# Kernel tuning notes

Measured on AMD Instinct MI355X. Metric: run time of the kernel, lower is better.

Reference implementation:

```python
import jax, jax.numpy as jnp
import numpy as np

B, N, D, K = 32, 4096, 256, 128


def setup_inputs() -> dict:
    key = jax.random.key(0)
    k1, k2, k3 = jax.random.split(key, 3)
    x = jax.random.normal(k1, (B, N, D), dtype=jnp.float32)
    # 'orthogonal' init proxy: unit-variance-ish codewords
    codewords = jax.random.normal(k2, (K, D), dtype=jnp.float32) / np.float32(np.sqrt(D))
    # keras 'uniform' initializer default range (-0.05, 0.05)
    scale = jax.random.uniform(k3, (K,), dtype=jnp.float32, minval=-0.05, maxval=0.05)
    return {"x": x, "codewords": codewords, "scale": scale}


def reference(x, codewords, scale):
    """Deep-TEN Encoding layer.

    scaledL2: w_ik = S_k * ||x_i - c_k||^2   (expanded, avoids (B,N,K,D) residuals)
    weights : W = softmax_k(w_ik)
    aggregate: E_k = sum_i W_ik * (x_i - c_k)
    """
    x2 = jnp.sum(x * x, axis=-1)                    # (B, N)
    c2 = jnp.sum(codewords * codewords, axis=-1)    # (K,)
    xc = jnp.einsum('bnd,kd->bnk', x, codewords)    # (B, N, K)
    sl2 = scale * (x2[..., None] - 2.0 * xc + c2)   # (B, N, K)
    W = jax.nn.softmax(sl2, axis=-1)                # softmax over codewords K
    # E_k = sum_i W_ik x_i - (sum_i W_ik) c_k
    E = jnp.einsum('bnk,bnd->bkd', W, x) - jnp.sum(W, axis=1)[..., None] * codewords
    return E  # (B, K, D)
```

## Files before the change

### kernel.cpp

```cpp
#include <hip/hip_runtime.h>

#define DEV __device__ __forceinline__

typedef __attribute__((ext_vector_type(8))) short bf16x8;
typedef __attribute__((ext_vector_type(4))) float f32x4;

constexpr int Nn = 4096, Dd = 256, Kk = 128;
constexpr int SEGS = 32;
constexpr int CH2  = 8;
constexpr int NCH  = Nn / CH2;
constexpr int NSTEP = 64;

DEV unsigned short f2bf(float f) {
  unsigned int u = __builtin_bit_cast(unsigned int, f);
  u += 0x7FFFu + ((u >> 16) & 1u);
  return (unsigned short)(u >> 16);
}
DEV float bf2f(unsigned short h) {
  unsigned int u = (unsigned int)h << 16;
  return __builtin_bit_cast(float, u);
}

DEV unsigned lds2(unsigned d, unsigned nbyte) {
  unsigned hh = (d & 7u) ^ ((d >> 4) & 7u) ^ (((d >> 7) & 1u) << 1);
  return d * 128u + (nbyte ^ (hh << 4));
}

DEV unsigned ldsc(unsigned row, unsigned byteInRow) {
  return row * 512u + (byteInRow ^ ((row & 7u) << 4));
}

DEV unsigned ldsw(unsigned k, unsigned nbyte) {
  unsigned h = (k & 7u) ^ (((k >> 3) & 1u) << 1);
  return k * 256u + (nbyte ^ (h << 4));
}

__global__ void enc_prep(const float* __restrict__ cw, const float* __restrict__ sc,
                         unsigned short* __restrict__ cbf, float2* __restrict__ tab,
                         float* __restrict__ Wsumg) {
  int k = blockIdx.x, l = threadIdx.x;
  float4 u = *(const float4*)(cw + k * Dd + l * 4);
  float s2 = u.x * u.x + u.y * u.y + u.z * u.z + u.w * u.w;
  #pragma unroll
  for (int o = 1; o < 64; o <<= 1) s2 += __shfl_xor(s2, o);
  unsigned short* dst = cbf + k * Dd + l * 4;
  dst[0] = f2bf(u.x); dst[1] = f2bf(u.y); dst[2] = f2bf(u.z); dst[3] = f2bf(u.w);
  if (l == 0) { float s = sc[k]; tab[k] = make_float2(s * s2, 2.0f * s); }
  if (l < 32) Wsumg[l * Kk + k] = 0.0f;
}

__global__ __launch_bounds__(512, 1) void enc_w(
    const float* __restrict__ x, const unsigned short* __restrict__ cbf,
    const float2* __restrict__ tab, unsigned short* __restrict__ Wt,
    float* __restrict__ Wsumg) {
  __shared__ __align__(16) char cL[65536];
  __shared__ float2 tabL[Kk];
  __shared__ float WsL[Kk];
  const int tid = threadIdx.x;
  const int w  = tid >> 6;
  const int l  = tid & 63;
  const int g  = l >> 4;
  const int ln = l & 15;

  {
    const int r = tid >> 2, part = tid & 3;
    const char* src = (const char*)cbf + r * 512 + part * 128;
    #pragma unroll
    for (int j = 0; j < 8; ++j) {
      float4 v = *(const float4*)(src + j * 16);
      *(float4*)(cL + ldsc((unsigned)r, (unsigned)(part * 128 + j * 16))) = v;
    }
  }
  if (tid < Kk) { tabL[tid] = tab[tid]; WsL[tid] = 0.0f; }
  __syncthreads();

  const int b   = blockIdx.x >> 5;
  const int seg = blockIdx.x & 31;
  const int nrow = seg * 128 + w * 16 + ln;
  const float* xrow = x + ((size_t)b * Nn + nrow) * Dd;

  f32x4 s1[8];
  const f32x4 zero4 = {0.f, 0.f, 0.f, 0.f};
  #pragma unroll
  for (int f = 0; f < 8; ++f) s1[f] = zero4;
  float x2p = 0.f;

  float4 pu[8][2];
  #pragma unroll
  for (int p = 0; p < 8; ++p) {
    pu[p][0] = *(const float4*)(xrow + p * 32 + g * 8);
    pu[p][1] = *(const float4*)(xrow + p * 32 + g * 8 + 4);
  }

  #pragma unroll
  for (int ks = 0; ks < 8; ++ks) {
    float4 u0 = pu[ks][0], u1 = pu[ks][1];
    x2p += u0.x*u0.x + u0.y*u0.y + u0.z*u0.z + u0.w*u0.w
         + u1.x*u1.x + u1.y*u1.y + u1.z*u1.z + u1.w*u1.w;
    bf16x8 xv;
    xv[0] = (short)f2bf(u0.x); xv[1] = (short)f2bf(u0.y);
    xv[2] = (short)f2bf(u0.z); xv[3] = (short)f2bf(u0.w);
    xv[4] = (short)f2bf(u1.x); xv[5] = (short)f2bf(u1.y);
    xv[6] = (short)f2bf(u1.z); xv[7] = (short)f2bf(u1.w);
    const unsigned colb = (unsigned)(ks * 64 + g * 16);
    #pragma unroll
    for (int f = 0; f < 8; ++f) {
      bf16x8 a = *(const bf16x8*)(cL + ldsc((unsigned)(f * 16 + ln), colb));
      s1[f] = __builtin_amdgcn_mfma_f32_16x16x32_bf16(a, xv, s1[f], 0, 0, 0);
    }
  }

  x2p += __shfl_xor(x2p, 16); x2p += __shfl_xor(x2p, 32);
  const float hx2 = 0.5f * x2p;
  float ssum = 0.f;
  #pragma unroll
  for (int f = 0; f < 8; ++f) {
    #pragma unroll
    for (int r = 0; r < 4; ++r) {
      const float2 ab = tabL[f * 16 + g * 4 + r];
      const float ev = __expf(ab.x + ab.y * (hx2 - s1[f][r]));
      s1[f][r] = ev;
      ssum += ev;
    }
  }
  ssum += __shfl_xor(ssum, 16); ssum += __shfl_xor(ssum, 32);
  const float rinv = 1.0f / ssum;

  __syncthreads();
  #pragma unroll
  for (int f = 0; f < 8; ++f) {
    #pragma unroll
    for (int r = 0; r < 4; ++r) {
      const int cwi = f * 16 + g * 4 + r;
      *(unsigned short*)(cL + ldsw((unsigned)cwi, (unsigned)((w * 16 + ln) * 2)))
          = f2bf(s1[f][r] * rinv);
    }
  }
  __syncthreads();
  {
    char* wq = (char*)(Wt + (size_t)b * Kk * Nn + seg * 128);
    #pragma unroll
    for (int j = 0; j < 4; ++j) {
      const unsigned o = (unsigned)tid * 16u + (unsigned)j * 8192u;
      const unsigned k = o >> 8, nb = o & 255u;
      float4 v = *(const float4*)(cL + ldsw(k, nb));
      *(float4*)(wq + (size_t)k * (Nn * 2) + nb) = v;
      const unsigned short* hv = (const unsigned short*)&v;
      float wsp = 0.f;
      #pragma unroll
      for (int q = 0; q < 8; ++q) wsp += bf2f(hv[q]);
      atomicAdd(&WsL[k], wsp);
    }
  }
  __syncthreads();
  if (tid < Kk) atomicAdd(&Wsumg[b * Kk + tid], WsL[tid]);
}

template<int PM>
__global__ __launch_bounds__(1024) void enc_e(
    const float* __restrict__ x, const unsigned short* __restrict__ Wt,
    unsigned short* __restrict__ Ep, float* __restrict__ out) {
  __shared__ __align__(16) char xs[2 * 32768];

  const int tid = threadIdx.x;
  const int w  = tid >> 6;
  const int l  = tid & 63;
  const int g  = l >> 4;
  const int ln = l & 15;
  const int wr = w >> 2, wc = w & 3;
  const int b  = blockIdx.x >> 3, ch = blockIdx.x & 7;

  const float* xb = x + ((size_t)b * Nn + ch * NCH) * Dd;
  const unsigned short* Wb = Wt + (size_t)b * Kk * Nn + ch * NCH;

  const int srow = w * 4 + g;
  const int sd0  = ln * 16;

  f32x4 acc[2][4];
  const f32x4 zero4 = {0.f, 0.f, 0.f, 0.f};
  #pragma unroll
  for (int mi = 0; mi < 2; ++mi)
    #pragma unroll
    for (int ni = 0; ni < 4; ++ni) acc[mi][ni] = zero4;

  {
    const float* p = xb + (size_t)srow * Dd + sd0;
    float4 u0 = *(const float4*)(p + 0), u1 = *(const float4*)(p + 4);
    float4 u2 = *(const float4*)(p + 8), u3 = *(const float4*)(p + 12);
    const float uu[16] = {u0.x,u0.y,u0.z,u0.w, u1.x,u1.y,u1.z,u1.w,
                          u2.x,u2.y,u2.z,u2.w, u3.x,u3.y,u3.z,u3.w};
    #pragma unroll
    for (int j = 0; j < 16; ++j)
      *(unsigned short*)(xs + lds2((unsigned)(sd0 + j), (unsigned)(srow * 2))) = f2bf(uu[j]);
  }
  bf16x8 wf[2][2];
  #pragma unroll
  for (int ks2 = 0; ks2 < 2; ++ks2)
    #pragma unroll
    for (int mi = 0; mi < 2; ++mi)
      wf[ks2][mi] = *(const bf16x8*)(Wb + (size_t)(wr * 32 + mi * 16 + ln) * Nn
                                        + ks2 * 32 + g * 8);
  __syncthreads();

  int cur = 0;
  for (int s = 0; s < CH2; ++s) {
    float4 n0, n1, n2, n3;
    bf16x8 wn[2][2];
    if (s + 1 < CH2) {
      const float* p = xb + (size_t)((s + 1) * NSTEP + srow) * Dd + sd0;
      n0 = *(const float4*)(p + 0); n1 = *(const float4*)(p + 4);
      n2 = *(const float4*)(p + 8); n3 = *(const float4*)(p + 12);
      #pragma unroll
      for (int ks2 = 0; ks2 < 2; ++ks2)
        #pragma unroll
        for (int mi = 0; mi < 2; ++mi)
          wn[ks2][mi] = *(const bf16x8*)(Wb + (size_t)(wr * 32 + mi * 16 + ln) * Nn
                                            + (s + 1) * NSTEP + ks2 * 32 + g * 8);
    }

    const char* xcur = xs + (cur << 15);
    #pragma unroll
    for (int ks2 = 0; ks2 < 2; ++ks2) {
      bf16x8 bg[4];
      #pragma unroll
      for (int ni = 0; ni < 4; ++ni)
        bg[ni] = *(const bf16x8*)(xcur + lds2((unsigned)(wc * 64 + ni * 16 + ln),
                                              (unsigned)((ks2 * 32 + g * 8) * 2)));
      #pragma unroll
      for (int mi = 0; mi < 2; ++mi)
        #pragma unroll
        for (int ni = 0; ni < 4; ++ni)
          acc[mi][ni] = __builtin_amdgcn_mfma_f32_16x16x32_bf16(wf[ks2][mi], bg[ni], acc[mi][ni], 0, 0, 0);
    }

    if (s + 1 < CH2) {
      char* xn = xs + ((cur ^ 1) << 15);
      const float uu[16] = {n0.x,n0.y,n0.z,n0.w, n1.x,n1.y,n1.z,n1.w,
                            n2.x,n2.y,n2.z,n2.w, n3.x,n3.y,n3.z,n3.w};
      #pragma unroll
      for (int j = 0; j < 16; ++j)
        *(unsigned short*)(xn + lds2((unsigned)(sd0 + j), (unsigned)(srow * 2))) = f2bf(uu[j]);
      #pragma unroll
      for (int ks2 = 0; ks2 < 2; ++ks2)
        #pragma unroll
        for (int mi = 0; mi < 2; ++mi)
          wf[ks2][mi] = wn[ks2][mi];
    }
    __syncthreads();
    cur ^= 1;
  }

  #pragma unroll
  for (int mi = 0; mi < 2; ++mi) {
    #pragma unroll
    for (int r = 0; r < 4; ++r) {
      const int k = wr * 32 + mi * 16 + g * 4 + r;
      #pragma unroll
      for (int ni = 0; ni < 4; ++ni) {
        const int d = wc * 64 + ni * 16 + ln;
        if (PM == 0) {
          Ep[(size_t)blockIdx.x * (Kk * Dd) + k * Dd + d] = f2bf(acc[mi][ni][r]);
        } else {
          atomicAdd(out + (size_t)b * (Kk * Dd) + k * Dd + d, acc[mi][ni][r]);
        }
      }
    }
  }
}

__global__ __launch_bounds__(256, 1) void enc_reduce_b16(
    const unsigned short* __restrict__ Ep, const float* __restrict__ Wsumg,
    const float* __restrict__ cw, float* __restrict__ out) {
  const size_t i = ((size_t)blockIdx.x * 256 + threadIdx.x) * 16;
  const int b   = (int)(i / (Kk * Dd));
  const int rem = (int)(i % (Kk * Dd));
  const int k   = rem >> 8;
  const unsigned short* p = Ep + (size_t)b * CH2 * (Kk * Dd) + rem;
  const float wsv = Wsumg[b * Kk + k];
  float sx[16];
  #pragma unroll
  for (int j = 0; j < 16; ++j) sx[j] = 0.f;
  #pragma unroll
  for (int c = 0; c < CH2; ++c) {
    const ushort4* q = (const ushort4*)(p + (size_t)c * (Kk * Dd));
    ushort4 v0 = q[0], v1 = q[1], v2 = q[2], v3 = q[3];
    sx[0]  += bf2f(v0.x); sx[1]  += bf2f(v0.y); sx[2]  += bf2f(v0.z); sx[3]  += bf2f(v0.w);
    sx[4]  += bf2f(v1.x); sx[5]  += bf2f(v1.y); sx[6]  += bf2f(v1.z); sx[7]  += bf2f(v1.w);
    sx[8]  += bf2f(v2.x); sx[9]  += bf2f(v2.y); sx[10] += bf2f(v2.z); sx[11] += bf2f(v2.w);
    sx[12] += bf2f(v3.x); sx[13] += bf2f(v3.y); sx[14] += bf2f(v3.z); sx[15] += bf2f(v3.w);
  }
  const float* cp = cw + (size_t)rem;
  float4 c0 = *(const float4*)(cp + 0), c1 = *(const float4*)(cp + 4);
  float4 c2 = *(const float4*)(cp + 8), c3 = *(const float4*)(cp + 12);
  float4* o = (float4*)(out + i);
  o[0] = make_float4(sx[0] - wsv * c0.x, sx[1] - wsv * c0.y, sx[2] - wsv * c0.z, sx[3] - wsv * c0.w);
  o[1] = make_float4(sx[4] - wsv * c1.x, sx[5] - wsv * c1.y, sx[6] - wsv * c1.z, sx[7] - wsv * c1.w);
  o[2] = make_float4(sx[8] - wsv * c2.x, sx[9] - wsv * c2.y, sx[10] - wsv * c2.z, sx[11] - wsv * c2.w);
  o[3] = make_float4(sx[12] - wsv * c3.x, sx[13] - wsv * c3.y, sx[14] - wsv * c3.z, sx[15] - wsv * c3.w);
}

__global__ __launch_bounds__(256, 1) void enc_fix(
    const float* __restrict__ Wsumg, const float* __restrict__ cw,
    float* __restrict__ out) {
  const size_t i = ((size_t)blockIdx.x * 256 + threadIdx.x) * 16;
  const int b   = (int)(i / (Kk * Dd));
  const int rem = (int)(i % (Kk * Dd));
  const int k   = rem >> 8;
  const float wsv = Wsumg[b * Kk + k];
  float* o = out + i;
  const float* cp = cw + (size_t)rem;
  #pragma unroll
  for (int j = 0; j < 16; ++j) o[j] -= wsv * cp[j];
}

extern "C" void kernel_launch(void* const* d_in, const int* in_sizes, int n_in,
                              void* d_out, int out_size, void* d_ws, size_t ws_size,
                              hipStream_t stream) {
  const float* x  = (const float*)d_in[0];
  const float* cw = (const float*)d_in[1];
  const float* sc = (const float*)d_in[2];
  float* out = (float*)d_out;

  unsigned short* cbf = (unsigned short*)d_ws;
  float2* tab = (float2*)((char*)d_ws + 65536);
  float*  Wsumg = (float*)((char*)d_ws + 66560);
  unsigned short* Wt = (unsigned short*)((char*)d_ws + 82944);
  unsigned short* Ep = (unsigned short*)((char*)d_ws + 82944 + (size_t)32 * Kk * Nn * 2);
  const size_t KD = (size_t)Kk * Dd;
  const size_t needFull = 82944 + (size_t)32 * Kk * Nn * 2 + (size_t)32 * CH2 * KD * 2;
  const size_t needAtm  = 82944 + (size_t)32 * Kk * Nn * 2;

  enc_prep<<<dim3(Kk), dim3(64), 0, stream>>>(cw, sc, cbf, tab, Wsumg);
  enc_w<<<dim3(32 * SEGS), dim3(512), 0, stream>>>(x, cbf, tab, Wt, Wsumg);

  if (ws_size >= needFull) {
    enc_e<0><<<dim3(32 * CH2), dim3(1024), 0, stream>>>(x, Wt, Ep, nullptr);
    enc_reduce_b16<<<dim3(256), dim3(256), 0, stream>>>(Ep, Wsumg, cw, out);
  } else if (ws_size >= needAtm) {
    hipMemsetAsync(d_out, 0, (size_t)out_size * sizeof(float), stream);
    enc_e<2><<<dim3(32 * CH2), dim3(1024), 0, stream>>>(x, Wt, nullptr, out);
    enc_fix<<<dim3(256), dim3(256), 0, stream>>>(Wsumg, cw, out);
  }
}
```

Measured before the change: 103.2 us.

## Move W column sums to a separate kernel and software-pipeline x loads in enc_w

Result: faster. 98.04 us (-5.0%).

```diff
diff --git a/kernel.cpp b/kernel.cpp
--- a/kernel.cpp
+++ b/kernel.cpp
@@ -36,8 +36,7 @@
 }
 
 __global__ void enc_prep(const float* __restrict__ cw, const float* __restrict__ sc,
-                         unsigned short* __restrict__ cbf, float2* __restrict__ tab,
-                         float* __restrict__ Wsumg) {
+                         unsigned short* __restrict__ cbf, float2* __restrict__ tab) {
   int k = blockIdx.x, l = threadIdx.x;
   float4 u = *(const float4*)(cw + k * Dd + l * 4);
   float s2 = u.x * u.x + u.y * u.y + u.z * u.z + u.w * u.w;
@@ -46,16 +45,13 @@
   unsigned short* dst = cbf + k * Dd + l * 4;
   dst[0] = f2bf(u.x); dst[1] = f2bf(u.y); dst[2] = f2bf(u.z); dst[3] = f2bf(u.w);
   if (l == 0) { float s = sc[k]; tab[k] = make_float2(s * s2, 2.0f * s); }
-  if (l < 32) Wsumg[l * Kk + k] = 0.0f;
 }
 
 __global__ __launch_bounds__(512, 1) void enc_w(
     const float* __restrict__ x, const unsigned short* __restrict__ cbf,
-    const float2* __restrict__ tab, unsigned short* __restrict__ Wt,
-    float* __restrict__ Wsumg) {
+    const float2* __restrict__ tab, unsigned short* __restrict__ Wt) {
   __shared__ __align__(16) char cL[65536];
   __shared__ float2 tabL[Kk];
-  __shared__ float WsL[Kk];
   const int tid = threadIdx.x;
   const int w  = tid >> 6;
   const int l  = tid & 63;
@@ -71,7 +67,7 @@
       *(float4*)(cL + ldsc((unsigned)r, (unsigned)(part * 128 + j * 16))) = v;
     }
   }
-  if (tid < Kk) { tabL[tid] = tab[tid]; WsL[tid] = 0.0f; }
+  if (tid < Kk) tabL[tid] = tab[tid];
   __syncthreads();
 
   const int b   = blockIdx.x >> 5;
@@ -85,16 +81,21 @@
   for (int f = 0; f < 8; ++f) s1[f] = zero4;
   float x2p = 0.f;
 
-  float4 pu[8][2];
-  #pragma unroll
-  for (int p = 0; p < 8; ++p) {
+  float4 pu[4][2];
+  #pragma unroll
+  for (int p = 0; p < 4; ++p) {
     pu[p][0] = *(const float4*)(xrow + p * 32 + g * 8);
     pu[p][1] = *(const float4*)(xrow + p * 32 + g * 8 + 4);
   }
+  __builtin_amdgcn_sched_barrier(0);
 
   #pragma unroll
   for (int ks = 0; ks < 8; ++ks) {
-    float4 u0 = pu[ks][0], u1 = pu[ks][1];
+    float4 u0 = pu[ks & 3][0], u1 = pu[ks & 3][1];
+    if (ks + 4 < 8) {
+      pu[ks & 3][0] = *(const float4*)(xrow + (ks + 4) * 32 + g * 8);
+      pu[ks & 3][1] = *(const float4*)(xrow + (ks + 4) * 32 + g * 8 + 4);
+    }
     x2p += u0.x*u0.x + u0.y*u0.y + u0.z*u0.z + u0.w*u0.w
          + u1.x*u1.x + u1.y*u1.y + u1.z*u1.z + u1.w*u1.w;
     bf16x8 xv;
@@ -108,6 +109,7 @@
       bf16x8 a = *(const bf16x8*)(cL + ldsc((unsigned)(f * 16 + ln), colb));
       s1[f] = __builtin_amdgcn_mfma_f32_16x16x32_bf16(a, xv, s1[f], 0, 0, 0);
     }
+    __builtin_amdgcn_sched_barrier(0);
   }
 
   x2p += __shfl_xor(x2p, 16); x2p += __shfl_xor(x2p, 32);
@@ -145,15 +147,26 @@
       const unsigned k = o >> 8, nb = o & 255u;
       float4 v = *(const float4*)(cL + ldsw(k, nb));
       *(float4*)(wq + (size_t)k * (Nn * 2) + nb) = v;
-      const unsigned short* hv = (const unsigned short*)&v;
-      float wsp = 0.f;
-      #pragma unroll
-      for (int q = 0; q < 8; ++q) wsp += bf2f(hv[q]);
-      atomicAdd(&WsL[k], wsp);
-    }
-  }
-  __syncthreads();
-  if (tid < Kk) atomicAdd(&Wsumg[b * Kk + tid], WsL[tid]);
+    }
+  }
+}
+
+__global__ __launch_bounds__(256, 1) void enc_wsum(
+    const unsigned short* __restrict__ Wt, float* __restrict__ Wsumg) {
+  const int w = threadIdx.x >> 6, l = threadIdx.x & 63;
+  const int row = blockIdx.x * 4 + w;
+  const unsigned short* p = Wt + (size_t)row * Nn + l * 8;
+  float s = 0.f;
+  #pragma unroll
+  for (int j = 0; j < 8; ++j) {
+    ushort4 v0 = *(const ushort4*)(p + j * 512);
+    ushort4 v1 = *(const ushort4*)(p + j * 512 + 4);
+    s += bf2f(v0.x) + bf2f(v0.y) + bf2f(v0.z) + bf2f(v0.w)
+       + bf2f(v1.x) + bf2f(v1.y) + bf2f(v1.z) + bf2f(v1.w);
+  }
+  #pragma unroll
+  for (int o = 1; o < 64; o <<= 1) s += __shfl_xor(s, o);
+  if (l == 0) Wsumg[row] = s;
 }
 
 template<int PM>
@@ -330,8 +343,9 @@
   const size_t needFull = 82944 + (size_t)32 * Kk * Nn * 2 + (size_t)32 * CH2 * KD * 2;
   const size_t needAtm  = 82944 + (size_t)32 * Kk * Nn * 2;
 
-  enc_prep<<<dim3(Kk), dim3(64), 0, stream>>>(cw, sc, cbf, tab, Wsumg);
-  enc_w<<<dim3(32 * SEGS), dim3(512), 0, stream>>>(x, cbf, tab, Wt, Wsumg);
+  enc_prep<<<dim3(Kk), dim3(64), 0, stream>>>(cw, sc, cbf, tab);
+  enc_w<<<dim3(32 * SEGS), dim3(512), 0, stream>>>(x, cbf, tab, Wt);
+  enc_wsum<<<dim3((32 * Kk) / 4), dim3(256), 0, stream>>>(Wt, Wsumg);
 
   if (ws_size >= needFull) {
     enc_e<0><<<dim3(32 * CH2), dim3(1024), 0, stream>>>(x, Wt, Ep, nullptr);
```
